# Kernel tuning notes

Measured on AMD Instinct MI355X. Metric: run time of the kernel, lower is better.

The kernel has to match this reference:

```python
import jax, jax.numpy as jnp
import numpy as np

N_NODE = 100000
N_EDGE = 1600000
D_IN = 128
D_OUT = 128
D_EDGE = 32
EPS = 1e-10


def setup_inputs() -> dict:
    key = jax.random.key(0)
    ks = jax.random.split(key, 8)
    x = jax.random.normal(ks[0], (N_NODE, D_IN), dtype=jnp.float32)
    edge_list = jax.random.randint(ks[1], (N_EDGE, 2), 0, N_NODE, dtype=jnp.int32)
    edge_weights = jax.random.uniform(ks[2], (N_EDGE,), dtype=jnp.float32)
    edge_feature = jax.random.normal(ks[3], (N_EDGE, D_EDGE), dtype=jnp.float32)
    W_lin = jax.random.normal(ks[4], (D_OUT, D_IN), dtype=jnp.float32) * 0.05
    b_lin = jnp.zeros((D_OUT,), dtype=jnp.float32)
    W_edge = jax.random.normal(ks[5], (D_IN, D_EDGE), dtype=jnp.float32) * 0.05
    b_edge = jnp.zeros((D_IN,), dtype=jnp.float32)
    return {"x": x, "edge_list": edge_list, "edge_weights": edge_weights,
            "edge_feature": edge_feature, "W_lin": W_lin, "b_lin": b_lin,
            "W_edge": W_edge, "b_edge": b_edge}


def reference(x, edge_list, edge_weights, edge_feature, W_lin, b_lin, W_edge, b_edge):
    N = x.shape[0]
    src = edge_list[:, 0]  # node_in
    dst = edge_list[:, 1]  # node_out
    loops = jnp.arange(N, dtype=src.dtype)
    node_in = jnp.concatenate([src, loops])    # [E+N]
    node_out = jnp.concatenate([dst, loops])   # [E+N]
    ew = jnp.concatenate([edge_weights, jnp.ones((N,), x.dtype)])  # [E+N]
    # weighted degrees (torchdrug convention) + 1 for self loops
    deg_in = jax.ops.segment_sum(edge_weights, src, num_segments=N) + 1.0
    deg_out = jax.ops.segment_sum(edge_weights, dst, num_segments=N) + 1.0
    # symmetric degree normalization per (extended) edge
    w = ew / (jnp.sqrt(deg_in[node_in] * deg_out[node_out]) + EPS)  # [E+N]
    # sparse adj.T @ x: gather source features, scale, scatter-add to dest
    update = jax.ops.segment_sum(w[:, None] * x[node_in], node_out, num_segments=N)
    # edge-feature contribution (zeros for self loops)
    e = edge_feature @ W_edge.T + b_edge                        # [E, D_IN]
    e = jnp.concatenate([e, jnp.zeros((N, e.shape[1]), x.dtype)])
    update = update + jax.ops.segment_sum(w[:, None] * e, node_out, num_segments=N)
    # combine: linear + relu
    return jax.nn.relu(update @ W_lin.T + b_lin)
```

## Files before the change

kernel.cpp:

```cpp
#include <hip/hip_runtime.h>

#define N_NODES 100000
#define N_EDGES 1600000
#define D 128
#define DE 32
#define SCAN_CHUNK 1024
#define N_CHUNKS ((N_NODES + SCAN_CHUNK - 1) / SCAN_CHUNK)
#define POS_BLOCKS (N_EDGES / 2 / 256)
#define XH_BLOCKS (N_NODES * D / 8 / 256)

typedef int v4i __attribute__((ext_vector_type(4)));
typedef __attribute__((ext_vector_type(8))) short bf16x8;
typedef __attribute__((ext_vector_type(4))) float f32x4;


__device__ inline float bflo(unsigned u) {
  return __uint_as_float(u << 16);
}
__device__ inline float bfhi(unsigned u) {
  return __uint_as_float(u & 0xFFFF0000u);
}
__device__ inline unsigned pk_bf2(float lo, float hi) {
  unsigned a = __float_as_uint(lo), b = __float_as_uint(hi);
  a = (a + 0x7FFFu + ((a >> 16) & 1)) >> 16;
  b = (b + 0x7FFFu + ((b >> 16) & 1)) >> 16;
  return a | (b << 16);
}

__global__ __launch_bounds__(256) void init_kernel(int* __restrict__ z) {
  int idx = blockIdx.x * 256 + threadIdx.x;
  if (idx < 5 * N_NODES) z[idx] = 0;
}

__global__ __launch_bounds__(256) void pre_kernel(
    const int4* __restrict__ el2, int* __restrict__ cursor,
    int2* __restrict__ pos2, const float4* __restrict__ x4,
    uint4* __restrict__ xh4) {
  int b = blockIdx.x;
  if (b < POS_BLOCKS) {
    int i = b * 256 + threadIdx.x;
    if (i >= N_EDGES / 2) return;
    int4 e = el2[i];
    int2 p;
    p.x = atomicAdd(&cursor[e.y], 1);
    p.y = atomicAdd(&cursor[e.w], 1);
    pos2[i] = p;
  } else {
    int i = (b - POS_BLOCKS) * 256 + threadIdx.x;
    if (i >= N_NODES * D / 8) return;
    float4 f0 = x4[2 * i], f1 = x4[2 * i + 1];
    uint4 o;
    o.x = pk_bf2(f0.x, f0.y);
    o.y = pk_bf2(f0.z, f0.w);
    o.z = pk_bf2(f1.x, f1.y);
    o.w = pk_bf2(f1.z, f1.w);
    xh4[i] = o;
  }
}

__global__ __launch_bounds__(256) void scan1_kernel(
    const int* __restrict__ counts, int* __restrict__ partial,
    int* __restrict__ blocksum) {
  __shared__ int lds[256];
  int t = threadIdx.x;
  int base = blockIdx.x * SCAN_CHUNK + t * 4;
  int c[4];
  int s = 0;
#pragma unroll
  for (int k = 0; k < 4; k++) {
    c[k] = (base + k < N_NODES) ? counts[base + k] : 0;
    s += c[k];
  }
  lds[t] = s;
  __syncthreads();
  for (int off = 1; off < 256; off <<= 1) {
    int tmp = (t >= off) ? lds[t - off] : 0;
    __syncthreads();
    lds[t] += tmp;
    __syncthreads();
  }
  int run = lds[t] - s;
#pragma unroll
  for (int k = 0; k < 4; k++) {
    int v = base + k;
    if (v < N_NODES) partial[v] = run;
    run += c[k];
  }
  if (t == 255) blocksum[blockIdx.x] = lds[255];
}

__global__ __launch_bounds__(128) void scan2_kernel(
    const int* __restrict__ blocksum, int* __restrict__ blockoff) {
  __shared__ int lds[128];
  int t = threadIdx.x;
  int v = (t < N_CHUNKS) ? blocksum[t] : 0;
  lds[t] = v;
  __syncthreads();
  for (int off = 1; off < 128; off <<= 1) {
    int tmp = (t >= off) ? lds[t - off] : 0;
    __syncthreads();
    lds[t] += tmp;
    __syncthreads();
  }
  if (t < N_CHUNKS) blockoff[t] = lds[t] - v;
}

__global__ __launch_bounds__(256) void place_kernel(
    const int4* __restrict__ el2, const float2* __restrict__ ew2,
    const int2* __restrict__ pos2, const int* __restrict__ partial,
    const int* __restrict__ blockoff, float* __restrict__ deg4,
    int4* __restrict__ rec) {
  int i = blockIdx.x * 256 + threadIdx.x;
  if (i >= N_EDGES / 2) return;
  int4 e = el2[i];
  float2 w = ew2[i];
  int2 p = pos2[i];
  int r0 = (threadIdx.x & 3) * N_NODES;
  atomicAdd(&deg4[r0 + e.x], w.x);
  atomicAdd(&deg4[r0 + e.z], w.y);
  int4 rA, rB;
  rA.x = e.x; rA.y = 2 * i;     rA.z = __float_as_int(w.x); rA.w = 0;
  rB.x = e.z; rB.y = 2 * i + 1; rB.z = __float_as_int(w.y); rB.w = 0;
  rec[partial[e.y] + blockoff[e.y >> 10] + p.x] = rA;
  rec[partial[e.w] + blockoff[e.w >> 10] + p.y] = rB;
}

__global__ __launch_bounds__(256) void rdi_kernel(
    const float* __restrict__ deg4, float* __restrict__ rdi) {
  int v = blockIdx.x * 256 + threadIdx.x;
  if (v >= N_NODES) return;
  rdi[v] = rsqrtf(1.f + deg4[v] + deg4[N_NODES + v] + deg4[2 * N_NODES + v] +
                  deg4[3 * N_NODES + v]);
}

template <bool XH16>
__global__ __launch_bounds__(256) void gather_fused_kernel(
    const float* __restrict__ x, const ushort* __restrict__ xh,
    const float* __restrict__ ef, const int* __restrict__ partial,
    const int* __restrict__ blockoff, const int* __restrict__ counts,
    const int4* __restrict__ rec, const float* __restrict__ rdi,
    const float* __restrict__ W_edge, const float* __restrict__ b_edge,
    float* __restrict__ out) {
  __shared__ __align__(16) float we[128 * 36];
  __shared__ float beS[128];
  int t = threadIdx.x;
#pragma unroll
  for (int i = 0; i < 4; ++i) {
    int f = t + i * 256;
    int r = f >> 3, kq = f & 7;
    *(float4*)&we[r * 36 + 4 * kq] = *(const float4*)&W_edge[r * DE + 4 * kq];
  }
  if (t < 128) beS[t] = b_edge[t];
  __syncthreads();

  int wid = t >> 6, lane = t & 63;
  int v = blockIdx.x * 4 + wid;
  if (v >= N_NODES) return;
  int start = partial[v] + blockoff[v >> 10];
  int cnt = counts[v];
  int lane31 = lane & 31;
  bool lowhalf = lane < 32;

  float A0 = 0.f, A1 = 0.f, B0 = 0.f, B1 = 0.f;
  float C0 = 0.f, C1 = 0.f, E0 = 0.f, E1 = 0.f;
  float ga = 0.f, gb = 0.f, gc = 0.f, gd = 0.f, dsum = 0.f, wsv = 0.f;

#define EFLOAD(eid) __builtin_nontemporal_load(&ef[(size_t)(eid)*DE + lane31])

  for (int base = 0; base < cnt; base += 64) {
    int nb = cnt - base;
    if (nb > 64) nb = 64;
    int s_l = 0, e_l = 0;
    float w_l = 0.f;
    if (lane < nb) {
      v4i rv = __builtin_nontemporal_load(
          (const v4i*)&rec[start + base + lane]);
      s_l = rv.x;
      e_l = rv.y;
      float wraw = __int_as_float(rv.z);
      w_l = wraw * rdi[s_l];
      dsum += wraw;
      wsv += w_l;
    }
    int i = 0;
    for (; i + 8 <= nb; i += 8) {
      int s0 = __shfl(s_l, i + 0), s1 = __shfl(s_l, i + 1);
      int s2 = __shfl(s_l, i + 2), s3 = __shfl(s_l, i + 3);
      int s4 = __shfl(s_l, i + 4), s5 = __shfl(s_l, i + 5);
      int s6 = __shfl(s_l, i + 6), s7 = __shfl(s_l, i + 7);
      float w0 = __shfl(w_l, i + 0), w1 = __shfl(w_l, i + 1);
      float w2 = __shfl(w_l, i + 2), w3 = __shfl(w_l, i + 3);
      float w4 = __shfl(w_l, i + 4), w5 = __shfl(w_l, i + 5);
      float w6 = __shfl(w_l, i + 6), w7 = __shfl(w_l, i + 7);
      int hh = lane >> 5;
      int eA = __shfl(e_l, i + 0 + hh), eB = __shfl(e_l, i + 2 + hh);
      int eC = __shfl(e_l, i + 4 + hh), eD = __shfl(e_l, i + 6 + hh);
      float wA = lowhalf ? w0 : w1, wB = lowhalf ? w2 : w3;
      float wC = lowhalf ? w4 : w5, wD = lowhalf ? w6 : w7;
      ga = fmaf(wA, EFLOAD(eA), ga);
      gb = fmaf(wB, EFLOAD(eB), gb);
      gc = fmaf(wC, EFLOAD(eC), gc);
      gd = fmaf(wD, EFLOAD(eD), gd);
      if (XH16) {
        unsigned u0 = ((const unsigned*)(xh + (size_t)s0 * D))[lane];
        unsigned u1 = ((const unsigned*)(xh + (size_t)s1 * D))[lane];
        unsigned u2 = ((const unsigned*)(xh + (size_t)s2 * D))[lane];
        unsigned u3 = ((const unsigned*)(xh + (size_t)s3 * D))[lane];
        unsigned u4 = ((const unsigned*)(xh + (size_t)s4 * D))[lane];
        unsigned u5 = ((const unsigned*)(xh + (size_t)s5 * D))[lane];
        unsigned u6 = ((const unsigned*)(xh + (size_t)s6 * D))[lane];
        unsigned u7 = ((const unsigned*)(xh + (size_t)s7 * D))[lane];
        A0 = fmaf(w0, bflo(u0), A0); A1 = fmaf(w0, bfhi(u0), A1);
        B0 = fmaf(w1, bflo(u1), B0); B1 = fmaf(w1, bfhi(u1), B1);
        C0 = fmaf(w2, bflo(u2), C0); C1 = fmaf(w2, bfhi(u2), C1);
        E0 = fmaf(w3, bflo(u3), E0); E1 = fmaf(w3, bfhi(u3), E1);
        A0 = fmaf(w4, bflo(u4), A0); A1 = fmaf(w4, bfhi(u4), A1);
        B0 = fmaf(w5, bflo(u5), B0); B1 = fmaf(w5, bfhi(u5), B1);
        C0 = fmaf(w6, bflo(u6), C0); C1 = fmaf(w6, bfhi(u6), C1);
        E0 = fmaf(w7, bflo(u7), E0); E1 = fmaf(w7, bfhi(u7), E1);
      } else {
        float2 u0 = ((const float2*)(x + (size_t)s0 * D))[lane];
        float2 u1 = ((const float2*)(x + (size_t)s1 * D))[lane];
        float2 u2 = ((const float2*)(x + (size_t)s2 * D))[lane];
        float2 u3 = ((const float2*)(x + (size_t)s3 * D))[lane];
        float2 u4 = ((const float2*)(x + (size_t)s4 * D))[lane];
        float2 u5 = ((const float2*)(x + (size_t)s5 * D))[lane];
        float2 u6 = ((const float2*)(x + (size_t)s6 * D))[lane];
        float2 u7 = ((const float2*)(x + (size_t)s7 * D))[lane];
        A0 = fmaf(w0, u0.x, A0); A1 = fmaf(w0, u0.y, A1);
        B0 = fmaf(w1, u1.x, B0); B1 = fmaf(w1, u1.y, B1);
        C0 = fmaf(w2, u2.x, C0); C1 = fmaf(w2, u2.y, C1);
        E0 = fmaf(w3, u3.x, E0); E1 = fmaf(w3, u3.y, E1);
        A0 = fmaf(w4, u4.x, A0); A1 = fmaf(w4, u4.y, A1);
        B0 = fmaf(w5, u5.x, B0); B1 = fmaf(w5, u5.y, B1);
        C0 = fmaf(w6, u6.x, C0); C1 = fmaf(w6, u6.y, C1);
        E0 = fmaf(w7, u7.x, E0); E1 = fmaf(w7, u7.y, E1);
      }
    }
    for (; i + 2 <= nb; i += 2) {
      int s0 = __shfl(s_l, i), s1 = __shfl(s_l, i + 1);
      float w0 = __shfl(w_l, i), w1 = __shfl(w_l, i + 1);
      int eE = __shfl(e_l, i + (lane >> 5));
      float wE = lowhalf ? w0 : w1;
      ga = fmaf(wE, EFLOAD(eE), ga);
      if (XH16) {
        unsigned u0 = ((const unsigned*)(xh + (size_t)s0 * D))[lane];
        unsigned u1 = ((const unsigned*)(xh + (size_t)s1 * D))[lane];
        A0 = fmaf(w0, bflo(u0), A0); A1 = fmaf(w0, bfhi(u0), A1);
        B0 = fmaf(w1, bflo(u1), B0); B1 = fmaf(w1, bfhi(u1), B1);
      } else {
        float2 u0 = ((const float2*)(x + (size_t)s0 * D))[lane];
        float2 u1 = ((const float2*)(x + (size_t)s1 * D))[lane];
        A0 = fmaf(w0, u0.x, A0); A1 = fmaf(w0, u0.y, A1);
        B0 = fmaf(w1, u1.x, B0); B1 = fmaf(w1, u1.y, B1);
      }
    }
    if (i < nb) {
      int s0 = __shfl(s_l, i);
      float w0 = __shfl(w_l, i);
      int eA = __shfl(e_l, i);
      if (lowhalf) ga = fmaf(w0, EFLOAD(eA), ga);
      if (XH16) {
        unsigned u0 = ((const unsigned*)(xh + (size_t)s0 * D))[lane];
        A0 = fmaf(w0, bflo(u0), A0);
        A1 = fmaf(w0, bfhi(u0), A1);
      } else {
        float2 u0 = ((const float2*)(x + (size_t)s0 * D))[lane];
        A0 = fmaf(w0, u0.x, A0);
        A1 = fmaf(w0, u0.y, A1);
      }
    }
  }
#undef EFLOAD
  float a0 = (A0 + B0) + (C0 + E0);
  float a1 = (A1 + B1) + (C1 + E1);
#pragma unroll
  for (int off = 32; off; off >>= 1) {
    dsum += __shfl_xor(dsum, off);
    wsv += __shfl_xor(wsv, off);
  }
  float rdo = rsqrtf(1.f + dsum);
  float gk = (ga + gb) + (gc + gd);
  gk += __shfl(gk, (lane + 32) & 63);

  int half = lane >> 1;
  float v0 = __shfl(a0, half), v1 = __shfl(a1, half);
  float accLo = (lane & 1) ? v1 : v0;
  float q0 = __shfl(a0, 32 + half), q1 = __shfl(a1, 32 + half);
  float accHi = (lane & 1) ? q1 : q0;

  size_t ro = (size_t)v * D;
  float xs0, xs1;
  if (XH16) {
    xs0 = __uint_as_float((unsigned)xh[ro + lane] << 16);
    xs1 = __uint_as_float((unsigned)xh[ro + lane + 64] << 16);
  } else {
    xs0 = x[ro + lane];
    xs1 = x[ro + lane + 64];
  }
  float rdiv = rdi[v];
  float s0 = accLo + rdiv * xs0 + wsv * beS[lane];
  float s1 = accHi + rdiv * xs1 + wsv * beS[lane + 64];
#pragma unroll
  for (int kq = 0; kq < 8; ++kq) {
    float4 w0 = *(const float4*)&we[lane * 36 + 4 * kq];
    float4 w1 = *(const float4*)&we[(lane + 64) * 36 + 4 * kq];
    float g0 = __shfl(gk, 4 * kq);
    float g1 = __shfl(gk, 4 * kq + 1);
    float g2 = __shfl(gk, 4 * kq + 2);
    float g3 = __shfl(gk, 4 * kq + 3);
    s0 += g0 * w0.x + g1 * w0.y + g2 * w0.z + g3 * w0.w;
    s1 += g0 * w1.x + g1 * w1.y + g2 * w1.z + g3 * w1.w;
  }
  out[ro + lane] = rdo * s0;
  out[ro + lane + 64] = rdo * s1;
}

__global__ __launch_bounds__(256) void gemm2_mfma_kernel(
    const float* __restrict__ W_lin, const float* __restrict__ b_lin,
    float* __restrict__ out) {
  __shared__ __align__(16) ushort Asb[128 * 40];
  __shared__ __align__(16) ushort Wsb[128 * 132];
  int t = threadIdx.x;
  int vbase = blockIdx.x * 128;

#pragma unroll
  for (int i = 0; i < 16; ++i) {
    int idx = t + i * 256;
    int r = idx >> 5;
    int c = (idx & 31) * 4;
    float4 f = *(const float4*)&W_lin[r * D + c];
    uint2 u;
    u.x = pk_bf2(f.x, f.y);
    u.y = pk_bf2(f.z, f.w);
    *(uint2*)&Wsb[r * 132 + c] = u;
  }

  int lane = t & 63, w = t >> 6;
  int l15 = lane & 15, kg = lane >> 4;
  f32x4 acc[2][8] = {};

  for (int ks = 0; ks < 4; ++ks) {
    __syncthreads();
#pragma unroll
    for (int i = 0; i < 4; ++i) {
      int idx = t + i * 256;
      int r = idx >> 3;
      int c = (idx & 7) * 4;
      float4 f = make_float4(0.f, 0.f, 0.f, 0.f);
      if (vbase + r < N_NODES)
        f = *(const float4*)&out[(size_t)(vbase + r) * D + ks * 32 + c];
      uint2 u;
      u.x = pk_bf2(f.x, f.y);
      u.y = pk_bf2(f.z, f.w);
      *(uint2*)&Asb[r * 40 + c] = u;
    }
    __syncthreads();
    bf16x8 a0 = *(const bf16x8*)&Asb[(w * 32 + l15) * 40 + kg * 8];
    bf16x8 a1 = *(const bf16x8*)&Asb[(w * 32 + 16 + l15) * 40 + kg * 8];
#pragma unroll
    for (int nt = 0; nt < 8; ++nt) {
      const ushort* bp = &Wsb[(nt * 16 + l15) * 132 + ks * 32 + kg * 8];
      uint2 q0 = *(const uint2*)bp;
      uint2 q1 = *(const uint2*)(bp + 4);
      uint4 bu = make_uint4(q0.x, q0.y, q1.x, q1.y);
      bf16x8 bf = *(bf16x8*)&bu;
      acc[0][nt] =
          __builtin_amdgcn_mfma_f32_16x16x32_bf16(a0, bf, acc[0][nt], 0, 0, 0);
      acc[1][nt] =
          __builtin_amdgcn_mfma_f32_16x16x32_bf16(a1, bf, acc[1][nt], 0, 0, 0);
    }
  }

#pragma unroll
  for (int nt = 0; nt < 8; ++nt) {
    int col = nt * 16 + l15;
    float bl = b_lin[col];
#pragma unroll
    for (int mt = 0; mt < 2; ++mt) {
#pragma unroll
      for (int j = 0; j < 4; ++j) {
        int row = vbase + w * 32 + mt * 16 + kg * 4 + j;
        if (row < N_NODES)
          out[(size_t)row * D + col] = fmaxf(acc[mt][nt][j] + bl, 0.f);
      }
    }
  }
}

extern "C" void kernel_launch(void* const* d_in, const int* in_sizes, int n_in,
                              void* d_out, int out_size, void* d_ws,
                              size_t ws_size, hipStream_t stream) {
  const float* x      = (const float*)d_in[0];
  const int*   el     = (const int*)d_in[1];
  const float* ew     = (const float*)d_in[2];
  const float* ef     = (const float*)d_in[3];
  const float* W_lin  = (const float*)d_in[4];
  const float* b_lin  = (const float*)d_in[5];
  const float* W_edge = (const float*)d_in[6];
  const float* b_edge = (const float*)d_in[7];

  float* outp = (float*)d_out;

  char* base = (char*)d_ws;
  size_t off = 0;
  int4* rec      = (int4*)(base + off); off += (size_t)N_EDGES * 16;
  ushort* xh     = (ushort*)(base + off); off += (size_t)N_NODES * D * 2;
  int*  pos      = (int*)(base + off);  off += (size_t)N_EDGES * 4;
  float* deg4    = (float*)(base + off); off += (size_t)4 * N_NODES * 4;
  int*  cursor   = (int*)(base + off);  off += (size_t)N_NODES * 4;
  int*  partial  = (int*)(base + off);  off += (size_t)N_NODES * 4;
  int*  blocksum = (int*)(base + off);  off += 512;
  int*  blockoff = (int*)(base + off);  off += 512;
  float* rdi     = (float*)(base + off); off += (size_t)N_NODES * 4;
  const size_t REQ_FAST = off;
  bool fast = (ws_size >= REQ_FAST);
  if (!fast) {
    off = (size_t)N_EDGES * 16;
    pos      = (int*)(base + off);  off += (size_t)N_EDGES * 4;
    deg4     = (float*)(base + off); off += (size_t)4 * N_NODES * 4;
    cursor   = (int*)(base + off);  off += (size_t)N_NODES * 4;
    partial  = (int*)(base + off);  off += (size_t)N_NODES * 4;
    blocksum = (int*)(base + off);  off += 512;
    blockoff = (int*)(base + off);  off += 512;
    rdi      = (float*)(base + off); off += (size_t)N_NODES * 4;
    xh       = nullptr;
  }

  hipLaunchKernelGGL(init_kernel, dim3((5 * N_NODES + 255) / 256), dim3(256),
                     0, stream, (int*)deg4);
  hipLaunchKernelGGL(pre_kernel, dim3(fast ? POS_BLOCKS + XH_BLOCKS
                                           : POS_BLOCKS),
                     dim3(256), 0, stream, (const int4*)el, cursor, (int2*)pos,
                     (const float4*)x, (uint4*)xh);
  hipLaunchKernelGGL(scan1_kernel, dim3(N_CHUNKS), dim3(256), 0, stream,
                     cursor, partial, blocksum);
  hipLaunchKernelGGL(scan2_kernel, dim3(1), dim3(128), 0, stream, blocksum,
                     blockoff);
  hipLaunchKernelGGL(place_kernel, dim3((N_EDGES / 2 + 255) / 256), dim3(256),
                     0, stream, (const int4*)el, (const float2*)ew,
                     (const int2*)pos, partial, blockoff, deg4, rec);
  hipLaunchKernelGGL(rdi_kernel, dim3((N_NODES + 255) / 256), dim3(256), 0,
                     stream, deg4, rdi);
  if (fast) {
    hipLaunchKernelGGL(gather_fused_kernel<true>, dim3((N_NODES + 3) / 4),
                       dim3(256), 0, stream, x, xh, ef, partial, blockoff,
                       cursor, rec, rdi, W_edge, b_edge, outp);
  } else {
    hipLaunchKernelGGL(gather_fused_kernel<false>, dim3((N_NODES + 3) / 4),
                       dim3(256), 0, stream, x, xh, ef, partial, blockoff,
                       cursor, rec, rdi, W_edge, b_edge, outp);
  }
  hipLaunchKernelGGL(gemm2_mfma_kernel, dim3((N_NODES + 127) / 128), dim3(256),
                     0, stream, W_lin, b_lin, outp);
}
```

Measured before the change: 356.1 us.

## Fold edge-feature projection into final GEMM via precombined W_lin·W_edge weights

```diff
diff --git a/kernel.cpp b/kernel.cpp
--- a/kernel.cpp
+++ b/kernel.cpp
@@ -133,25 +133,48 @@
                   deg4[3 * N_NODES + v]);
 }
 
-template <bool XH16>
+__global__ __launch_bounds__(256) void combo_kernel(
+    const float* __restrict__ W_lin, const float* __restrict__ W_edge,
+    const float* __restrict__ b_edge, float* __restrict__ wcombo,
+    float* __restrict__ blbe) {
+  int idx = blockIdx.x * 256 + threadIdx.x;
+  int j = idx >> 5, k = idx & 31;
+  float s = 0.f;
+#pragma unroll 8
+  for (int d = 0; d < D; ++d) s += W_lin[j * D + d] * W_edge[d * DE + k];
+  wcombo[j * DE + k] = s;
+  if (blockIdx.x == 0 && threadIdx.x < D) {
+    int jj = threadIdx.x;
+    float b = 0.f;
+#pragma unroll 8
+    for (int d = 0; d < D; ++d) b += W_lin[jj * D + d] * b_edge[d];
+    blbe[jj] = b;
+  }
+}
+
+template <bool XH16, bool FUSEWE>
 __global__ __launch_bounds__(256) void gather_fused_kernel(
     const float* __restrict__ x, const ushort* __restrict__ xh,
     const float* __restrict__ ef, const int* __restrict__ partial,
     const int* __restrict__ blockoff, const int* __restrict__ counts,
     const int4* __restrict__ rec, const float* __restrict__ rdi,
     const float* __restrict__ W_edge, const float* __restrict__ b_edge,
+    float* __restrict__ gs, float* __restrict__ csc,
     float* __restrict__ out) {
-  __shared__ __align__(16) float we[128 * 36];
-  __shared__ float beS[128];
+  __shared__ __align__(16) float we[FUSEWE ? 128 * 36 : 4];
+  __shared__ float beS[FUSEWE ? 128 : 4];
   int t = threadIdx.x;
-#pragma unroll
-  for (int i = 0; i < 4; ++i) {
-    int f = t + i * 256;
-    int r = f >> 3, kq = f & 7;
-    *(float4*)&we[r * 36 + 4 * kq] = *(const float4*)&W_edge[r * DE + 4 * kq];
-  }
-  if (t < 128) beS[t] = b_edge[t];
-  __syncthreads();
+  if (FUSEWE) {
+#pragma unroll
+    for (int i = 0; i < 4; ++i) {
+      int f = t + i * 256;
+      int r = f >> 3, kq = f & 7;
+      *(float4*)&we[r * 36 + 4 * kq] =
+          *(const float4*)&W_edge[r * DE + 4 * kq];
+    }
+    if (t < 128) beS[t] = b_edge[t];
+    __syncthreads();
+  }
 
   int wid = t >> 6, lane = t & 63;
   int v = blockIdx.x * 4 + wid;
@@ -283,13 +306,35 @@
   float gk = (ga + gb) + (gc + gd);
   gk += __shfl(gk, (lane + 32) & 63);
 
+  size_t ro = (size_t)v * D;
+  float rdiv = rdi[v];
+
+  if (!FUSEWE) {
+    float xs0, xs1;
+    if (XH16) {
+      unsigned u = ((const unsigned*)(xh + ro))[lane];
+      xs0 = bflo(u);
+      xs1 = bfhi(u);
+    } else {
+      float2 u = ((const float2*)(x + ro))[lane];
+      xs0 = u.x;
+      xs1 = u.y;
+    }
+    float2 st;
+    st.x = rdo * (a0 + rdiv * xs0);
+    st.y = rdo * (a1 + rdiv * xs1);
+    ((float2*)(out + ro))[lane] = st;
+    if (lowhalf) gs[(size_t)v * DE + lane] = rdo * gk;
+    if (lane == 0) csc[v] = rdo * wsv;
+    return;
+  }
+
   int half = lane >> 1;
   float v0 = __shfl(a0, half), v1 = __shfl(a1, half);
   float accLo = (lane & 1) ? v1 : v0;
   float q0 = __shfl(a0, 32 + half), q1 = __shfl(a1, 32 + half);
   float accHi = (lane & 1) ? q1 : q0;
 
-  size_t ro = (size_t)v * D;
   float xs0, xs1;
   if (XH16) {
     xs0 = __uint_as_float((unsigned)xh[ro + lane] << 16);
@@ -298,7 +343,6 @@
     xs0 = x[ro + lane];
     xs1 = x[ro + lane + 64];
   }
-  float rdiv = rdi[v];
   float s0 = accLo + rdiv * xs0 + wsv * beS[lane];
   float s1 = accHi + rdiv * xs1 + wsv * beS[lane + 64];
 #pragma unroll
@@ -316,11 +360,15 @@
   out[ro + lane + 64] = rdo * s1;
 }
 
+template <bool EXT>
 __global__ __launch_bounds__(256) void gemm2_mfma_kernel(
     const float* __restrict__ W_lin, const float* __restrict__ b_lin,
+    const float* __restrict__ wcombo, const float* __restrict__ blbe,
+    const float* __restrict__ gs, const float* __restrict__ csc,
     float* __restrict__ out) {
   __shared__ __align__(16) ushort Asb[128 * 40];
   __shared__ __align__(16) ushort Wsb[128 * 132];
+  __shared__ __align__(16) ushort Csb[128 * 36];
   int t = threadIdx.x;
   int vbase = blockIdx.x * 128;
 
@@ -335,12 +383,26 @@
     u.y = pk_bf2(f.z, f.w);
     *(uint2*)&Wsb[r * 132 + c] = u;
   }
+  if (EXT) {
+#pragma unroll
+    for (int i = 0; i < 4; ++i) {
+      int idx = t + i * 256;
+      int r = idx >> 3;
+      int c = (idx & 7) * 4;
+      float4 f = *(const float4*)&wcombo[r * DE + c];
+      uint2 u;
+      u.x = pk_bf2(f.x, f.y);
+      u.y = pk_bf2(f.z, f.w);
+      *(uint2*)&Csb[r * 36 + c] = u;
+    }
+  }
 
   int lane = t & 63, w = t >> 6;
   int l15 = lane & 15, kg = lane >> 4;
   f32x4 acc[2][8] = {};
 
-  for (int ks = 0; ks < 4; ++ks) {
+  const int KSTEPS = EXT ? 5 : 4;
+  for (int ks = 0; ks < KSTEPS; ++ks) {
     __syncthreads();
 #pragma unroll
     for (int i = 0; i < 4; ++i) {
@@ -348,8 +410,12 @@
       int r = idx >> 3;
       int c = (idx & 7) * 4;
       float4 f = make_float4(0.f, 0.f, 0.f, 0.f);
-      if (vbase + r < N_NODES)
-        f = *(const float4*)&out[(size_t)(vbase + r) * D + ks * 32 + c];
+      if (vbase + r < N_NODES) {
+        if (!EXT || ks < 4)
+          f = *(const float4*)&out[(size_t)(vbase + r) * D + ks * 32 + c];
+        else
+          f = *(const float4*)&gs[(size_t)(vbase + r) * DE + c];
+      }
       uint2 u;
       u.x = pk_bf2(f.x, f.y);
       u.y = pk_bf2(f.z, f.w);
@@ -360,9 +426,16 @@
     bf16x8 a1 = *(const bf16x8*)&Asb[(w * 32 + 16 + l15) * 40 + kg * 8];
 #pragma unroll
     for (int nt = 0; nt < 8; ++nt) {
-      const ushort* bp = &Wsb[(nt * 16 + l15) * 132 + ks * 32 + kg * 8];
-      uint2 q0 = *(const uint2*)bp;
-      uint2 q1 = *(const uint2*)(bp + 4);
+      uint2 q0, q1;
+      if (!EXT || ks < 4) {
+        const ushort* bp = &Wsb[(nt * 16 + l15) * 132 + ks * 32 + kg * 8];
+        q0 = *(const uint2*)bp;
+        q1 = *(const uint2*)(bp + 4);
+      } else {
+        const ushort* bp = &Csb[(nt * 16 + l15) * 36 + kg * 8];
+        q0 = *(const uint2*)bp;
+        q1 = *(const uint2*)(bp + 4);
+      }
       uint4 bu = make_uint4(q0.x, q0.y, q1.x, q1.y);
       bf16x8 bf = *(bf16x8*)&bu;
       acc[0][nt] =
@@ -376,13 +449,17 @@
   for (int nt = 0; nt < 8; ++nt) {
     int col = nt * 16 + l15;
     float bl = b_lin[col];
+    float bb = EXT ? blbe[col] : 0.f;
 #pragma unroll
     for (int mt = 0; mt < 2; ++mt) {
 #pragma unroll
       for (int j = 0; j < 4; ++j) {
         int row = vbase + w * 32 + mt * 16 + kg * 4 + j;
-        if (row < N_NODES)
-          out[(size_t)row * D + col] = fmaxf(acc[mt][nt][j] + bl, 0.f);
+        if (row < N_NODES) {
+          float val = acc[mt][nt][j] + bl;
+          if (EXT) val += csc[row] * bb;
+          out[(size_t)row * D + col] = fmaxf(val, 0.f);
+        }
       }
     }
   }
@@ -413,9 +490,14 @@
   int*  blocksum = (int*)(base + off);  off += 512;
   int*  blockoff = (int*)(base + off);  off += 512;
   float* rdi     = (float*)(base + off); off += (size_t)N_NODES * 4;
-  const size_t REQ_FAST = off;
-  bool fast = (ws_size >= REQ_FAST);
-  if (!fast) {
+  const size_t REQ1 = off;
+  float* gsbuf   = (float*)(base + off); off += (size_t)N_NODES * DE * 4;
+  float* csc     = (float*)(base + off); off += (size_t)N_NODES * 4;
+  float* wcombo  = (float*)(base + off); off += (size_t)D * DE * 4;
+  float* blbe    = (float*)(base + off); off += 512;
+  const size_t REQ2 = off;
+  int tier = (ws_size >= REQ2) ? 2 : (ws_size >= REQ1) ? 1 : 0;
+  if (tier == 0) {
     off = (size_t)N_EDGES * 16;
     pos      = (int*)(base + off);  off += (size_t)N_EDGES * 4;
     deg4     = (float*)(base + off); off += (size_t)4 * N_NODES * 4;
@@ -429,8 +511,8 @@
 
   hipLaunchKernelGGL(init_kernel, dim3((5 * N_NODES + 255) / 256), dim3(256),
                      0, stream, (int*)deg4);
-  hipLaunchKernelGGL(pre_kernel, dim3(fast ? POS_BLOCKS + XH_BLOCKS
-                                           : POS_BLOCKS),
+  hipLaunchKernelGGL(pre_kernel,
+                     dim3(tier ? POS_BLOCKS + XH_BLOCKS : POS_BLOCKS),
                      dim3(256), 0, stream, (const int4*)el, cursor, (int2*)pos,
                      (const float4*)x, (uint4*)xh);
   hipLaunchKernelGGL(scan1_kernel, dim3(N_CHUNKS), dim3(256), 0, stream,
@@ -442,15 +524,33 @@
                      (const int2*)pos, partial, blockoff, deg4, rec);
   hipLaunchKernelGGL(rdi_kernel, dim3((N_NODES + 255) / 256), dim3(256), 0,
                      stream, deg4, rdi);
-  if (fast) {
-    hipLaunchKernelGGL(gather_fused_kernel<true>, dim3((N_NODES + 3) / 4),
-                       dim3(256), 0, stream, x, xh, ef, partial, blockoff,
-                       cursor, rec, rdi, W_edge, b_edge, outp);
+  if (tier == 2) {
+    hipLaunchKernelGGL(combo_kernel, dim3(16), dim3(256), 0, stream, W_lin,
+                       W_edge, b_edge, wcombo, blbe);
+    hipLaunchKernelGGL((gather_fused_kernel<true, false>),
+                       dim3((N_NODES + 3) / 4), dim3(256), 0, stream, x, xh,
+                       ef, partial, blockoff, cursor, rec, rdi, W_edge,
+                       b_edge, gsbuf, csc, outp);
+    hipLaunchKernelGGL(gemm2_mfma_kernel<true>, dim3((N_NODES + 127) / 128),
+                       dim3(256), 0, stream, W_lin, b_lin, wcombo, blbe,
+                       gsbuf, csc, outp);
+  } else if (tier == 1) {
+    hipLaunchKernelGGL((gather_fused_kernel<true, true>),
+                       dim3((N_NODES + 3) / 4), dim3(256), 0, stream, x, xh,
+                       ef, partial, blockoff, cursor, rec, rdi, W_edge,
+                       b_edge, (float*)nullptr, (float*)nullptr, outp);
+    hipLaunchKernelGGL(gemm2_mfma_kernel<false>, dim3((N_NODES + 127) / 128),
+                       dim3(256), 0, stream, W_lin, b_lin, (const float*)nullptr,
+                       (const float*)nullptr, (const float*)nullptr,
+                       (const float*)nullptr, outp);
   } else {
-    hipLaunchKernelGGL(gather_fused_kernel<false>, dim3((N_NODES + 3) / 4),
-                       dim3(256), 0, stream, x, xh, ef, partial, blockoff,
-                       cursor, rec, rdi, W_edge, b_edge, outp);
-  }
-  hipLaunchKernelGGL(gemm2_mfma_kernel, dim3((N_NODES + 127) / 128), dim3(256),
-                     0, stream, W_lin, b_lin, outp);
-}
+    hipLaunchKernelGGL((gather_fused_kernel<false, true>),
+                       dim3((N_NODES + 3) / 4), dim3(256), 0, stream, x, xh,
+                       ef, partial, blockoff, cursor, rec, rdi, W_edge,
+                       b_edge, (float*)nullptr, (float*)nullptr, outp);
+    hipLaunchKernelGGL(gemm2_mfma_kernel<false>, dim3((N_NODES + 127) / 128),
+                       dim3(256), 0, stream, W_lin, b_lin, (const float*)nullptr,
+                       (const float*)nullptr, (const float*)nullptr,
+                       (const float*)nullptr, outp);
+  }
+}
```

After: 342.3 us. 3.9% less time.
